# Kernel tuning notes

Hardware: AMD Instinct MI355X
Metric: run time of the kernel (lower is better)

Reference implementation:

```python
import jax, jax.numpy as jnp
import numpy as np

T, H, I, E, TOPK = 2048, 2048, 1408, 8, 2


def setup_inputs() -> dict:
    key = jax.random.key(0)
    k1, k2, k3, k4 = jax.random.split(key, 4)
    x = jax.random.normal(k1, (T, H), dtype=jnp.float32)
    router_logits = jax.random.normal(k2, (T, E), dtype=jnp.float32)
    # scale weights down so activations stay well-conditioned
    w13_weight = jax.random.normal(k3, (E, 2 * I, H), dtype=jnp.float32) * (1.0 / np.sqrt(H))
    w2_weight = jax.random.normal(k4, (E, H, I), dtype=jnp.float32) * (1.0 / np.sqrt(I))
    return {"x": x, "router_logits": router_logits, "w13_weight": w13_weight,
            "w2_weight": w2_weight, "top_k": TOPK}


def reference(x, router_logits, w13_weight, w2_weight, top_k):
    # --- select_experts: softmax scoring, top-k, renormalize ---
    probs = jax.nn.softmax(router_logits.astype(jnp.float32), axis=-1)   # [T, E]
    topk_w, topk_ids = jax.lax.top_k(probs, top_k)                        # [T, k]
    topk_w = topk_w / jnp.sum(topk_w, axis=-1, keepdims=True)             # renormalize
    topk_w = topk_w.astype(x.dtype)

    n_tok = x.shape[0]
    n_exp = w13_weight.shape[0]
    inter = w2_weight.shape[2]

    # dense combine weights [T, E]: zero for unselected experts
    comb = jnp.zeros((n_tok, n_exp), dtype=x.dtype)
    comb = comb.at[jnp.arange(n_tok)[:, None], topk_ids].add(topk_w)

    # --- fused_experts: gated SiLU MLP per expert, weighted combine ---
    gate_up = jnp.einsum('th,eih->tei', x, w13_weight)                    # [T, E, 2I]
    gate, up = gate_up[..., :inter], gate_up[..., inter:]
    act = jax.nn.silu(gate) * up                                          # [T, E, I]
    out = jnp.einsum('tei,ehi,te->th', act, w2_weight, comb)              # [T, H]
    return out
```

## Files before the change

### kernel.cpp

```cpp
#include <hip/hip_runtime.h>
#include <hip/hip_bf16.h>
#include <stdint.h>

#define T_TOK 2048
#define H_DIM 2048
#define I_DIM 1408
#define NEXP  8
#define NPOS  4096
#define NPAD  5120
#define MAXT  40

typedef short short8 __attribute__((ext_vector_type(8)));
typedef float f32x4  __attribute__((ext_vector_type(4)));

__device__ __forceinline__ short f2bf(float f) {
  union { float f; uint32_t u; } v; v.f = f;
  uint32_t r = (v.u + 0x7FFFu + ((v.u >> 16) & 1u)) >> 16;
  return (short)r;
}

__device__ __forceinline__ short8 cvt8(f32x4 a, f32x4 b) {
  __hip_bfloat162 h0 = __float22bfloat162_rn(float2{a[0], a[1]});
  __hip_bfloat162 h1 = __float22bfloat162_rn(float2{a[2], a[3]});
  __hip_bfloat162 h2 = __float22bfloat162_rn(float2{b[0], b[1]});
  __hip_bfloat162 h3 = __float22bfloat162_rn(float2{b[2], b[3]});
  short2 s0, s1, s2, s3;
  __builtin_memcpy(&s0, &h0, 4); __builtin_memcpy(&s1, &h1, 4);
  __builtin_memcpy(&s2, &h2, 4); __builtin_memcpy(&s3, &h3, 4);
  short8 r;
  r[0] = s0.x; r[1] = s0.y; r[2] = s1.x; r[3] = s1.y;
  r[4] = s2.x; r[5] = s2.y; r[6] = s3.x; r[7] = s3.y;
  return r;
}

__device__ __forceinline__ void load_lds16(const void* g, void* l) {
  __builtin_amdgcn_global_load_lds((const __attribute__((address_space(1))) uint32_t*)g,
                                   (__attribute__((address_space(3))) uint32_t*)l,
                                   16, 0, 0);
}

__global__ void k_routing(const float* __restrict__ logits,
                          int* __restrict__ pos_token,
                          float* __restrict__ pos_w,
                          int* __restrict__ eoff,
                          int* __restrict__ inv) {
  __shared__ int   s_ids[T_TOK];
  __shared__ float s_w0[T_TOK];
  __shared__ float s_w1[T_TOK];
  __shared__ int s_cnt[NEXP], s_cur[NEXP], s_off[NEXP + 1];
  const int tid = threadIdx.x;
  if (tid < NEXP) { s_cnt[tid] = 0; s_cur[tid] = 0; }
  for (int p = tid; p < NPAD; p += blockDim.x) { pos_token[p] = 0; pos_w[p] = 0.f; }
  __syncthreads();

  for (int t = tid; t < T_TOK; t += blockDim.x) {
    float l[NEXP];
#pragma unroll
    for (int e = 0; e < NEXP; ++e) l[e] = logits[t * NEXP + e];
    int b0 = 0; float v0 = l[0];
#pragma unroll
    for (int e = 1; e < NEXP; ++e) if (l[e] > v0) { v0 = l[e]; b0 = e; }
    int b1 = -1; float v1 = -1e30f;
#pragma unroll
    for (int e = 0; e < NEXP; ++e) if (e != b0 && l[e] > v1) { v1 = l[e]; b1 = e; }
    float t1 = __expf(v1 - v0);
    float w0 = 1.f / (1.f + t1);
    float w1 = 1.f - w0;
    s_ids[t] = b0 | (b1 << 8);
    s_w0[t] = w0; s_w1[t] = w1;
    atomicAdd(&s_cnt[b0], 1);
    atomicAdd(&s_cnt[b1], 1);
  }
  __syncthreads();
  if (tid == 0) {
    int acc = 0;
    for (int e = 0; e < NEXP; ++e) {
      s_off[e] = acc;
      acc += (s_cnt[e] + 127) & ~127;
    }
    s_off[NEXP] = acc;
    for (int e = 0; e <= NEXP; ++e) eoff[e] = s_off[e];
  }
  __syncthreads();
  for (int t = tid; t < T_TOK; t += blockDim.x) {
    int ids = s_ids[t];
    int e0 = ids & 255, e1 = ids >> 8;
    int p0 = s_off[e0] + atomicAdd(&s_cur[e0], 1);
    pos_token[p0] = t; pos_w[p0] = s_w0[t];
    int p1 = s_off[e1] + atomicAdd(&s_cur[e1], 1);
    pos_token[p1] = t; pos_w[p1] = s_w1[t];
    inv[2 * t] = p0; inv[2 * t + 1] = p1;
  }
}

__global__ void k_gather(const float* __restrict__ x,
                         const int* __restrict__ pos_token,
                         short* __restrict__ xg) {
  const int p = blockIdx.x;
  const int tid = threadIdx.x;
  const int tok = pos_token[p];
  const f32x4* src = (const f32x4*)(x + (size_t)tok * H_DIM);
  f32x4 a = src[tid * 2];
  f32x4 b = src[tid * 2 + 1];
  ((short8*)(xg + (size_t)p * H_DIM))[tid] = cvt8(a, b);
}

__device__ __forceinline__ int tile_expert(const int* eoff, int row0) {
  int e = 0;
#pragma unroll
  for (int i = 1; i < NEXP; ++i) if (row0 >= eoff[i]) e = i;
  return e;
}

__global__ __launch_bounds__(256, 3) void k_gateup(
    const short* __restrict__ xg, const float* __restrict__ w13,
    const int* __restrict__ eoff, short* __restrict__ act) {
  __shared__ __align__(16) short a_s[2][128 * 32];
  __shared__ __align__(16) short bg_s[2][64 * 32];
  __shared__ __align__(16) short bu_s[2][64 * 32];

  int bxr = blockIdx.x;
  const int bx = (bxr & 7) * 110 + (bxr >> 3);
  const int tile = bx / 22;
  const int nt = bx - tile * 22;
  const int row0 = tile * 128;
  if (row0 >= eoff[NEXP]) return;
  const int e = tile_expert(eoff, row0);

  const int tid = threadIdx.x;
  const int wid = tid >> 6;
  const int lane = tid & 63;
  const int wm = wid >> 1, wn = wid & 1;

  f32x4 accg[4][2] = {};
  f32x4 accu[4][2] = {};

  const short* aG  = xg + (size_t)row0 * H_DIM;
  const float* bgG = w13 + (size_t)e * (2 * I_DIM) * H_DIM + (size_t)(nt * 64) * H_DIM;
  const float* buG = bgG + (size_t)I_DIM * H_DIM;

  const int row  = tid >> 2;
  const int scol = ((tid & 3) ^ ((tid >> 3) & 3)) * 8;

  auto stageA = [&](int t, int bi) {
    const int ks = t * 32;
    load_lds16(aG + (size_t)row * H_DIM + ks + scol,        (char*)a_s[bi] + wid * 1024);
    load_lds16(aG + (size_t)(64 + row) * H_DIM + ks + scol, (char*)a_s[bi] + 4096 + wid * 1024);
  };
  auto ldB = [&](int t, f32x4& g0, f32x4& g1, f32x4& u0, f32x4& u1) {
    const int ks = t * 32;
    const float* sg = bgG + (size_t)row * H_DIM + ks + scol;
    const float* su = buG + (size_t)row * H_DIM + ks + scol;
    g0 = *(const f32x4*)sg; g1 = *(const f32x4*)(sg + 4);
    u0 = *(const f32x4*)su; u1 = *(const f32x4*)(su + 4);
  };
  auto wrB = [&](int bi, f32x4& g0, f32x4& g1, f32x4& u0, f32x4& u1) {
    *(short8*)((char*)bg_s[bi] + tid * 16) = cvt8(g0, g1);
    *(short8*)((char*)bu_s[bi] + tid * 16) = cvt8(u0, u1);
  };

  auto compute = [&](int bi) {
    const int asl = ((lane >> 4) ^ ((lane >> 1) & 3)) * 16;
    short8 af[4];
#pragma unroll
    for (int fm = 0; fm < 4; ++fm) {
      int m = wm * 64 + fm * 16 + (lane & 15);
      af[fm] = *(const short8*)((const char*)a_s[bi] + m * 64 + asl);
    }
#pragma unroll
    for (int fn = 0; fn < 2; ++fn) {
      int n = wn * 32 + fn * 16 + (lane & 15);
      short8 bg = *(const short8*)((const char*)bg_s[bi] + n * 64 + asl);
      short8 bu = *(const short8*)((const char*)bu_s[bi] + n * 64 + asl);
#pragma unroll
      for (int fm = 0; fm < 4; ++fm)
        accg[fm][fn] = __builtin_amdgcn_mfma_f32_16x16x32_bf16(af[fm], bg, accg[fm][fn], 0, 0, 0);
#pragma unroll
      for (int fm = 0; fm < 4; ++fm)
        accu[fm][fn] = __builtin_amdgcn_mfma_f32_16x16x32_bf16(af[fm], bu, accu[fm][fn], 0, 0, 0);
    }
  };

  const int NK = H_DIM / 32;
  f32x4 g0e, g1e, u0e, u1e, g0o, g1o, u0o, u1o;

  stageA(0, 0);
  ldB(0, g0e, g1e, u0e, u1e);
  wrB(0, g0e, g1e, u0e, u1e);
  ldB(1, g0e, g1e, u0e, u1e);
  ldB(2, g0o, g1o, u0o, u1o);
  __syncthreads();

#define GU_STEP(T, G0, G1, U0, U1)                                            \
  {                                                                           \
    const int t_ = (T);                                                       \
    const int bi_ = t_ & 1;                                                   \
    const int tn_ = (t_ + 1 < NK) ? t_ + 1 : NK - 1;                          \
    const int tf_ = (t_ + 3 < NK) ? t_ + 3 : NK - 1;                          \
    stageA(tn_, bi_ ^ 1);                                                     \
    __builtin_amdgcn_sched_barrier(0);                                        \
    wrB(bi_ ^ 1, G0, G1, U0, U1);                                             \
    ldB(tf_, G0, G1, U0, U1);                                                 \
    compute(bi_);                                                             \
    asm volatile("s_waitcnt vmcnt(4) lgkmcnt(0)" ::: "memory");               \
    __builtin_amdgcn_s_barrier();                                             \
  }
  for (int tp = 0; tp < NK; tp += 2) {
    GU_STEP(tp,     g0e, g1e, u0e, u1e);
    GU_STEP(tp + 1, g0o, g1o, u0o, u1o);
  }
#undef GU_STEP
  asm volatile("s_waitcnt vmcnt(0)" ::: "memory");

#pragma unroll
  for (int fm = 0; fm < 4; ++fm) {
#pragma unroll
    for (int rr = 0; rr < 4; ++rr) {
      int m = wm * 64 + fm * 16 + (lane >> 4) * 4 + rr;
      size_t grow = (size_t)(row0 + m);
#pragma unroll
      for (int fn = 0; fn < 2; ++fn) {
        int col = nt * 64 + wn * 32 + fn * 16 + (lane & 15);
        float g = accg[fm][fn][rr];
        float u = accu[fm][fn][rr];
        float a = g / (1.f + __expf(-g)) * u;
        act[grow * I_DIM + col] = f2bf(a);
      }
    }
  }
}

__global__ __launch_bounds__(256, 3) void k_down(
    const short* __restrict__ act, const float* __restrict__ w2,
    const int* __restrict__ eoff, float* __restrict__ y) {
  __shared__ __align__(16) short a_s[2][128 * 32];
  __shared__ __align__(16) short b_s[2][128 * 32];

  int bxr = blockIdx.x;
  const int bx = (bxr & 7) * 80 + (bxr >> 3);
  const int tile = bx >> 4;
  const int nt = bx & 15;
  const int row0 = tile * 128;
  if (row0 >= eoff[NEXP]) return;
  const int e = tile_expert(eoff, row0);

  const int tid = threadIdx.x;
  const int wid = tid >> 6;
  const int lane = tid & 63;
  const int wm = wid >> 1, wn = wid & 1;

  f32x4 acc[4][4] = {};

  const short* aG = act + (size_t)row0 * I_DIM;
  const float* bG = w2 + (size_t)e * H_DIM * I_DIM + (size_t)(nt * 128) * I_DIM;

  const int row  = tid >> 2;
  const int scol = ((tid & 3) ^ ((tid >> 3) & 3)) * 8;

  auto stageA = [&](int t, int bi) {
    const int ks = t * 32;
    load_lds16(aG + (size_t)row * I_DIM + ks + scol,        (char*)a_s[bi] + wid * 1024);
    load_lds16(aG + (size_t)(64 + row) * I_DIM + ks + scol, (char*)a_s[bi] + 4096 + wid * 1024);
  };
  auto ldB = [&](int t, f32x4& b00, f32x4& b01, f32x4& b10, f32x4& b11) {
    const int ks = t * 32;
    const float* s0 = bG + (size_t)row * I_DIM + ks + scol;
    const float* s1 = bG + (size_t)(64 + row) * I_DIM + ks + scol;
    b00 = *(const f32x4*)s0; b01 = *(const f32x4*)(s0 + 4);
    b10 = *(const f32x4*)s1; b11 = *(const f32x4*)(s1 + 4);
  };
  auto wrB = [&](int bi, f32x4& b00, f32x4& b01, f32x4& b10, f32x4& b11) {
    *(short8*)((char*)b_s[bi] + tid * 16)        = cvt8(b00, b01);
    *(short8*)((char*)b_s[bi] + 4096 + tid * 16) = cvt8(b10, b11);
  };

  auto compute = [&](int bi) {
    const int asl = ((lane >> 4) ^ ((lane >> 1) & 3)) * 16;
    short8 af[4];
#pragma unroll
    for (int fm = 0; fm < 4; ++fm) {
      int m = wm * 64 + fm * 16 + (lane & 15);
      af[fm] = *(const short8*)((const char*)a_s[bi] + m * 64 + asl);
    }
#pragma unroll
    for (int fn = 0; fn < 4; ++fn) {
      int n = wn * 64 + fn * 16 + (lane & 15);
      short8 bb = *(const short8*)((const char*)b_s[bi] + n * 64 + asl);
#pragma unroll
      for (int fm = 0; fm < 4; ++fm)
        acc[fm][fn] = __builtin_amdgcn_mfma_f32_16x16x32_bf16(af[fm], bb, acc[fm][fn], 0, 0, 0);
    }
  };

  const int NK = I_DIM / 32;
  f32x4 e0, e1, e2, e3, o0, o1, o2, o3;

  stageA(0, 0);
  ldB(0, e0, e1, e2, e3);
  wrB(0, e0, e1, e2, e3);
  ldB(1, e0, e1, e2, e3);
  ldB(2, o0, o1, o2, o3);
  __syncthreads();

#define DN_STEP(T, B0, B1, B2, B3)                                            \
  {                                                                           \
    const int t_ = (T);                                                       \
    const int bi_ = t_ & 1;                                                   \
    const int tn_ = (t_ + 1 < NK) ? t_ + 1 : NK - 1;                          \
    const int tf_ = (t_ + 3 < NK) ? t_ + 3 : NK - 1;                          \
    stageA(tn_, bi_ ^ 1);                                                     \
    __builtin_amdgcn_sched_barrier(0);                                        \
    wrB(bi_ ^ 1, B0, B1, B2, B3);                                             \
    ldB(tf_, B0, B1, B2, B3);                                                 \
    compute(bi_);                                                             \
    asm volatile("s_waitcnt vmcnt(4) lgkmcnt(0)" ::: "memory");               \
    __builtin_amdgcn_s_barrier();                                             \
  }
  for (int tp = 0; tp < NK; tp += 2) {
    DN_STEP(tp,     e0, e1, e2, e3);
    DN_STEP(tp + 1, o0, o1, o2, o3);
  }
#undef DN_STEP
  asm volatile("s_waitcnt vmcnt(0)" ::: "memory");

#pragma unroll
  for (int fm = 0; fm < 4; ++fm) {
#pragma unroll
    for (int rr = 0; rr < 4; ++rr) {
      int m = wm * 64 + fm * 16 + (lane >> 4) * 4 + rr;
      size_t grow = (size_t)(row0 + m);
#pragma unroll
      for (int fn = 0; fn < 4; ++fn) {
        int col = nt * 128 + wn * 64 + fn * 16 + (lane & 15);
        y[grow * H_DIM + col] = acc[fm][fn][rr];
      }
    }
  }
}

__global__ void k_combine(const float* __restrict__ y,
                          const int* __restrict__ inv,
                          const float* __restrict__ pos_w,
                          float* __restrict__ out) {
  const int t = blockIdx.x;
  const int tid = threadIdx.x;
  const int p0 = inv[2 * t], p1 = inv[2 * t + 1];
  const float w0 = pos_w[p0], w1 = pos_w[p1];
  const float4* y0 = (const float4*)(y + (size_t)p0 * H_DIM);
  const float4* y1 = (const float4*)(y + (size_t)p1 * H_DIM);
  float4* o = (float4*)(out + (size_t)t * H_DIM);
#pragma unroll
  for (int i = 0; i < 2; ++i) {
    float4 a = y0[tid * 2 + i];
    float4 b = y1[tid * 2 + i];
    float4 r;
    r.x = w0 * a.x + w1 * b.x;
    r.y = w0 * a.y + w1 * b.y;
    r.z = w0 * a.z + w1 * b.z;
    r.w = w0 * a.w + w1 * b.w;
    o[tid * 2 + i] = r;
  }
}

extern "C" void kernel_launch(void* const* d_in, const int* in_sizes, int n_in,
                              void* d_out, int out_size, void* d_ws, size_t ws_size,
                              hipStream_t stream) {
  const float* x      = (const float*)d_in[0];
  const float* logits = (const float*)d_in[1];
  const float* w13    = (const float*)d_in[2];
  const float* w2     = (const float*)d_in[3];
  (void)in_sizes; (void)n_in; (void)out_size; (void)ws_size;
  float* out = (float*)d_out;
  char* ws = (char*)d_ws;

  size_t o = 0;
  auto alloc = [&](size_t bytes) { size_t r = o; o += (bytes + 255) & ~(size_t)255; return r; };
  short* xg        = (short*)(ws + alloc((size_t)NPAD * H_DIM * 2));
  short* act       = (short*)(ws + alloc((size_t)NPAD * I_DIM * 2));
  float* y         = (float*)(ws + alloc((size_t)NPAD * H_DIM * 4));
  int*   pos_token = (int*)  (ws + alloc((size_t)NPAD * 4));
  float* pos_w     = (float*)(ws + alloc((size_t)NPAD * 4));
  int*   inv       = (int*)  (ws + alloc((size_t)T_TOK * 2 * 4));
  int*   eoff      = (int*)  (ws + alloc((NEXP + 1) * 4));

  k_routing<<<1, 1024, 0, stream>>>(logits, pos_token, pos_w, eoff, inv);
  k_gather<<<NPAD, 256, 0, stream>>>(x, pos_token, xg);
  k_gateup<<<MAXT * 22, 256, 0, stream>>>(xg, w13, eoff, act);
  k_down<<<MAXT * 16, 256, 0, stream>>>(act, w2, eoff, y);
  k_combine<<<T_TOK, 256, 0, stream>>>(y, inv, pos_w, out);
}
```

Before: 216.0 us.

## Triple-buffer A tiles with two-stage prefetch and regroup block-to-tile mapping

Both MoE GEMM kernels now keep three LDS buffers for the activation (A) tile and issue its direct-to-LDS loads two k-steps ahead instead of one, relaxing the vmcnt wait so more global loads stay in flight. This targets exposed latency on the A-tile loads. The block-index mapping is also changed so each group of eight consecutive blocks shares an n-tile across five row tiles, aiming at better L2 reuse of weight tiles. The cost is extra LDS per block, which may reduce occupancy, and the modulo-3 buffer indexing adds address arithmetic.

Result: slower. 237.0 us (+9.7%).

```diff
diff --git a/kernel.cpp b/kernel.cpp
--- a/kernel.cpp
+++ b/kernel.cpp
@@ -115,14 +115,15 @@
 __global__ __launch_bounds__(256, 3) void k_gateup(
     const short* __restrict__ xg, const float* __restrict__ w13,
     const int* __restrict__ eoff, short* __restrict__ act) {
-  __shared__ __align__(16) short a_s[2][128 * 32];
+  __shared__ __align__(16) short a_s[3][128 * 32];
   __shared__ __align__(16) short bg_s[2][64 * 32];
   __shared__ __align__(16) short bu_s[2][64 * 32];
 
-  int bxr = blockIdx.x;
-  const int bx = (bxr & 7) * 110 + (bxr >> 3);
-  const int tile = bx / 22;
-  const int nt = bx - tile * 22;
+  const int bxr = blockIdx.x;
+  const int c = bxr & 7;
+  const int l = bxr >> 3;
+  const int nt = l / 5;
+  const int tile = c * 5 + (l % 5);
   const int row0 = tile * 128;
   if (row0 >= eoff[NEXP]) return;
   const int e = tile_expert(eoff, row0);
@@ -142,10 +143,10 @@
   const int row  = tid >> 2;
   const int scol = ((tid & 3) ^ ((tid >> 3) & 3)) * 8;
 
-  auto stageA = [&](int t, int bi) {
+  auto stageA = [&](int t, int ai) {
     const int ks = t * 32;
-    load_lds16(aG + (size_t)row * H_DIM + ks + scol,        (char*)a_s[bi] + wid * 1024);
-    load_lds16(aG + (size_t)(64 + row) * H_DIM + ks + scol, (char*)a_s[bi] + 4096 + wid * 1024);
+    load_lds16(aG + (size_t)row * H_DIM + ks + scol,        (char*)a_s[ai] + wid * 1024);
+    load_lds16(aG + (size_t)(64 + row) * H_DIM + ks + scol, (char*)a_s[ai] + 4096 + wid * 1024);
   };
   auto ldB = [&](int t, f32x4& g0, f32x4& g1, f32x4& u0, f32x4& u1) {
     const int ks = t * 32;
@@ -159,13 +160,13 @@
     *(short8*)((char*)bu_s[bi] + tid * 16) = cvt8(u0, u1);
   };
 
-  auto compute = [&](int bi) {
+  auto compute = [&](int ai, int bi) {
     const int asl = ((lane >> 4) ^ ((lane >> 1) & 3)) * 16;
     short8 af[4];
 #pragma unroll
     for (int fm = 0; fm < 4; ++fm) {
       int m = wm * 64 + fm * 16 + (lane & 15);
-      af[fm] = *(const short8*)((const char*)a_s[bi] + m * 64 + asl);
+      af[fm] = *(const short8*)((const char*)a_s[ai] + m * 64 + asl);
     }
 #pragma unroll
     for (int fn = 0; fn < 2; ++fn) {
@@ -187,27 +188,29 @@
   stageA(0, 0);
   ldB(0, g0e, g1e, u0e, u1e);
   wrB(0, g0e, g1e, u0e, u1e);
-  ldB(1, g0e, g1e, u0e, u1e);
-  ldB(2, g0o, g1o, u0o, u1o);
+  stageA(1, 1);
+  ldB(1, g0o, g1o, u0o, u1o);
+  ldB(2, g0e, g1e, u0e, u1e);
   __syncthreads();
 
 #define GU_STEP(T, G0, G1, U0, U1)                                            \
   {                                                                           \
     const int t_ = (T);                                                       \
+    const int ai_ = t_ % 3;                                                   \
     const int bi_ = t_ & 1;                                                   \
-    const int tn_ = (t_ + 1 < NK) ? t_ + 1 : NK - 1;                          \
+    const int ta_ = (t_ + 2 < NK) ? t_ + 2 : NK - 1;                          \
     const int tf_ = (t_ + 3 < NK) ? t_ + 3 : NK - 1;                          \
-    stageA(tn_, bi_ ^ 1);                                                     \
+    stageA(ta_, (t_ + 2) % 3);                                                \
     __builtin_amdgcn_sched_barrier(0);                                        \
     wrB(bi_ ^ 1, G0, G1, U0, U1);                                             \
     ldB(tf_, G0, G1, U0, U1);                                                 \
-    compute(bi_);                                                             \
-    asm volatile("s_waitcnt vmcnt(4) lgkmcnt(0)" ::: "memory");               \
+    compute(ai_, bi_);                                                        \
+    asm volatile("s_waitcnt vmcnt(6) lgkmcnt(0)" ::: "memory");               \
     __builtin_amdgcn_s_barrier();                                             \
   }
   for (int tp = 0; tp < NK; tp += 2) {
-    GU_STEP(tp,     g0e, g1e, u0e, u1e);
-    GU_STEP(tp + 1, g0o, g1o, u0o, u1o);
+    GU_STEP(tp,     g0o, g1o, u0o, u1o);
+    GU_STEP(tp + 1, g0e, g1e, u0e, u1e);
   }
 #undef GU_STEP
   asm volatile("s_waitcnt vmcnt(0)" ::: "memory");
@@ -233,13 +236,14 @@
 __global__ __launch_bounds__(256, 3) void k_down(
     const short* __restrict__ act, const float* __restrict__ w2,
     const int* __restrict__ eoff, float* __restrict__ y) {
-  __shared__ __align__(16) short a_s[2][128 * 32];
+  __shared__ __align__(16) short a_s[3][128 * 32];
   __shared__ __align__(16) short b_s[2][128 * 32];
 
-  int bxr = blockIdx.x;
-  const int bx = (bxr & 7) * 80 + (bxr >> 3);
-  const int tile = bx >> 4;
-  const int nt = bx & 15;
+  const int bxr = blockIdx.x;
+  const int c = bxr & 7;
+  const int l = bxr >> 3;
+  const int nt = l / 5;
+  const int tile = c * 5 + (l % 5);
   const int row0 = tile * 128;
   if (row0 >= eoff[NEXP]) return;
   const int e = tile_expert(eoff, row0);
@@ -257,10 +261,10 @@
   const int row  = tid >> 2;
   const int scol = ((tid & 3) ^ ((tid >> 3) & 3)) * 8;
 
-  auto stageA = [&](int t, int bi) {
+  auto stageA = [&](int t, int ai) {
     const int ks = t * 32;
-    load_lds16(aG + (size_t)row * I_DIM + ks + scol,        (char*)a_s[bi] + wid * 1024);
-    load_lds16(aG + (size_t)(64 + row) * I_DIM + ks + scol, (char*)a_s[bi] + 4096 + wid * 1024);
+    load_lds16(aG + (size_t)row * I_DIM + ks + scol,        (char*)a_s[ai] + wid * 1024);
+    load_lds16(aG + (size_t)(64 + row) * I_DIM + ks + scol, (char*)a_s[ai] + 4096 + wid * 1024);
   };
   auto ldB = [&](int t, f32x4& b00, f32x4& b01, f32x4& b10, f32x4& b11) {
     const int ks = t * 32;
@@ -274,13 +278,13 @@
     *(short8*)((char*)b_s[bi] + 4096 + tid * 16) = cvt8(b10, b11);
   };
 
-  auto compute = [&](int bi) {
+  auto compute = [&](int ai, int bi) {
     const int asl = ((lane >> 4) ^ ((lane >> 1) & 3)) * 16;
     short8 af[4];
 #pragma unroll
     for (int fm = 0; fm < 4; ++fm) {
       int m = wm * 64 + fm * 16 + (lane & 15);
-      af[fm] = *(const short8*)((const char*)a_s[bi] + m * 64 + asl);
+      af[fm] = *(const short8*)((const char*)a_s[ai] + m * 64 + asl);
     }
 #pragma unroll
     for (int fn = 0; fn < 4; ++fn) {
@@ -298,27 +302,29 @@
   stageA(0, 0);
   ldB(0, e0, e1, e2, e3);
   wrB(0, e0, e1, e2, e3);
-  ldB(1, e0, e1, e2, e3);
-  ldB(2, o0, o1, o2, o3);
+  stageA(1, 1);
+  ldB(1, o0, o1, o2, o3);
+  ldB(2, e0, e1, e2, e3);
   __syncthreads();
 
 #define DN_STEP(T, B0, B1, B2, B3)                                            \
   {                                                                           \
     const int t_ = (T);                                                       \
+    const int ai_ = t_ % 3;                                                   \
     const int bi_ = t_ & 1;                                                   \
-    const int tn_ = (t_ + 1 < NK) ? t_ + 1 : NK - 1;                          \
+    const int ta_ = (t_ + 2 < NK) ? t_ + 2 : NK - 1;                          \
     const int tf_ = (t_ + 3 < NK) ? t_ + 3 : NK - 1;                          \
-    stageA(tn_, bi_ ^ 1);                                                     \
+    stageA(ta_, (t_ + 2) % 3);                                                \
     __builtin_amdgcn_sched_barrier(0);                                        \
     wrB(bi_ ^ 1, B0, B1, B2, B3);                                             \
     ldB(tf_, B0, B1, B2, B3);                                                 \
-    compute(bi_);                                                             \
-    asm volatile("s_waitcnt vmcnt(4) lgkmcnt(0)" ::: "memory");               \
+    compute(ai_, bi_);                                                        \
+    asm volatile("s_waitcnt vmcnt(6) lgkmcnt(0)" ::: "memory");               \
     __builtin_amdgcn_s_barrier();                                             \
   }
   for (int tp = 0; tp < NK; tp += 2) {
-    DN_STEP(tp,     e0, e1, e2, e3);
-    DN_STEP(tp + 1, o0, o1, o2, o3);
+    DN_STEP(tp,     o0, o1, o2, o3);
+    DN_STEP(tp + 1, e0, e1, e2, e3);
   }
 #undef DN_STEP
   asm volatile("s_waitcnt vmcnt(0)" ::: "memory");
```

## Process two row tiles per gate-up block and simplify the prefetch pipeline

Applied to the files above, without the earlier changes.

The gate-up kernel now launches half as many blocks, and each block loops over two consecutive 128-row tiles while keeping the same weight column slice, so the block count roughly matches a single wave of CUs. The deep register prefetch of B three steps ahead, with manual waitcnt and s_barrier, is replaced by a plain one-step double buffer using __syncthreads. The aim is less tail imbalance and some weight reuse in L2 within a block. The cost is less latency hiding in the main loop, and tiles that span two experts load a different weight slice per half.

New measurement: 250.6 us. 1.16x slower.

```diff
diff --git a/kernel.cpp b/kernel.cpp
--- a/kernel.cpp
+++ b/kernel.cpp
@@ -5,10 +5,12 @@
 #define T_TOK 2048
 #define H_DIM 2048
 #define I_DIM 1408
+#define GU_W  2816
 #define NEXP  8
 #define NPOS  4096
 #define NPAD  5120
 #define MAXT  40
+#define NPAIR 20
 
 typedef short short8 __attribute__((ext_vector_type(8)));
 typedef float f32x4  __attribute__((ext_vector_type(4)));
@@ -120,113 +122,100 @@
   __shared__ __align__(16) short bu_s[2][64 * 32];
 
   int bxr = blockIdx.x;
-  const int bx = (bxr & 7) * 110 + (bxr >> 3);
-  const int tile = bx / 22;
-  const int nt = bx - tile * 22;
-  const int row0 = tile * 128;
-  if (row0 >= eoff[NEXP]) return;
-  const int e = tile_expert(eoff, row0);
+  const int bx = (bxr & 7) * 55 + (bxr >> 3);
+  const int c  = bx / 22;
+  const int nt = bx - c * 22;
 
   const int tid = threadIdx.x;
   const int wid = tid >> 6;
   const int lane = tid & 63;
   const int wm = wid >> 1, wn = wid & 1;
 
-  f32x4 accg[4][2] = {};
-  f32x4 accu[4][2] = {};
-
-  const short* aG  = xg + (size_t)row0 * H_DIM;
-  const float* bgG = w13 + (size_t)e * (2 * I_DIM) * H_DIM + (size_t)(nt * 64) * H_DIM;
-  const float* buG = bgG + (size_t)I_DIM * H_DIM;
-
   const int row  = tid >> 2;
   const int scol = ((tid & 3) ^ ((tid >> 3) & 3)) * 8;
 
-  auto stageA = [&](int t, int bi) {
-    const int ks = t * 32;
-    load_lds16(aG + (size_t)row * H_DIM + ks + scol,        (char*)a_s[bi] + wid * 1024);
-    load_lds16(aG + (size_t)(64 + row) * H_DIM + ks + scol, (char*)a_s[bi] + 4096 + wid * 1024);
-  };
-  auto ldB = [&](int t, f32x4& g0, f32x4& g1, f32x4& u0, f32x4& u1) {
-    const int ks = t * 32;
-    const float* sg = bgG + (size_t)row * H_DIM + ks + scol;
-    const float* su = buG + (size_t)row * H_DIM + ks + scol;
-    g0 = *(const f32x4*)sg; g1 = *(const f32x4*)(sg + 4);
-    u0 = *(const f32x4*)su; u1 = *(const f32x4*)(su + 4);
-  };
-  auto wrB = [&](int bi, f32x4& g0, f32x4& g1, f32x4& u0, f32x4& u1) {
-    *(short8*)((char*)bg_s[bi] + tid * 16) = cvt8(g0, g1);
-    *(short8*)((char*)bu_s[bi] + tid * 16) = cvt8(u0, u1);
-  };
-
-  auto compute = [&](int bi) {
-    const int asl = ((lane >> 4) ^ ((lane >> 1) & 3)) * 16;
-    short8 af[4];
+  for (int half = 0; half < 2; ++half) {
+    const int tile = c * 2 + half;
+    const int row0 = tile * 128;
+    if (row0 >= eoff[NEXP]) break;
+    const int e = tile_expert(eoff, row0);
+
+    f32x4 accg[4][2] = {};
+    f32x4 accu[4][2] = {};
+
+    const short* aG  = xg + (size_t)row0 * H_DIM;
+    const float* bgG = w13 + (size_t)e * GU_W * H_DIM + (size_t)(nt * 64) * H_DIM;
+    const float* buG = bgG + (size_t)I_DIM * H_DIM;
+
+    auto stageA = [&](int t, int bi) {
+      const int ks = t * 32;
+      load_lds16(aG + (size_t)row * H_DIM + ks + scol,        (char*)a_s[bi] + wid * 1024);
+      load_lds16(aG + (size_t)(64 + row) * H_DIM + ks + scol, (char*)a_s[bi] + 4096 + wid * 1024);
+    };
+
+    f32x4 g0, g1, u0, u1;
+    auto ldB = [&](int t) {
+      const int ks = t * 32;
+      const float* sg = bgG + (size_t)row * H_DIM + ks + scol;
+      const float* su = buG + (size_t)row * H_DIM + ks + scol;
+      g0 = *(const f32x4*)sg; g1 = *(const f32x4*)(sg + 4);
+      u0 = *(const f32x4*)su; u1 = *(const f32x4*)(su + 4);
+    };
+    auto wrB = [&](int bi) {
+      *(short8*)((char*)bg_s[bi] + tid * 16) = cvt8(g0, g1);
+      *(short8*)((char*)bu_s[bi] + tid * 16) = cvt8(u0, u1);
+    };
+
+    auto compute = [&](int bi) {
+      const int asl = ((lane >> 4) ^ ((lane >> 1) & 3)) * 16;
+      short8 af[4];
+#pragma unroll
+      for (int fm = 0; fm < 4; ++fm) {
+        int m = wm * 64 + fm * 16 + (lane & 15);
+        af[fm] = *(const short8*)((const char*)a_s[bi] + m * 64 + asl);
+      }
+#pragma unroll
+      for (int fn = 0; fn < 2; ++fn) {
+        int n = wn * 32 + fn * 16 + (lane & 15);
+        short8 bg = *(const short8*)((const char*)bg_s[bi] + n * 64 + asl);
+        short8 bu = *(const short8*)((const char*)bu_s[bi] + n * 64 + asl);
+#pragma unroll
+        for (int fm = 0; fm < 4; ++fm)
+          accg[fm][fn] = __builtin_amdgcn_mfma_f32_16x16x32_bf16(af[fm], bg, accg[fm][fn], 0, 0, 0);
+#pragma unroll
+        for (int fm = 0; fm < 4; ++fm)
+          accu[fm][fn] = __builtin_amdgcn_mfma_f32_16x16x32_bf16(af[fm], bu, accu[fm][fn], 0, 0, 0);
+      }
+    };
+
+    const int NK = H_DIM / 32;
+    stageA(0, 0); ldB(0); wrB(0);
+    __syncthreads();
+    for (int t = 0; t < NK; ++t) {
+      int bi = t & 1;
+      if (t + 1 < NK) { stageA(t + 1, bi ^ 1); ldB(t + 1); }
+      compute(bi);
+      if (t + 1 < NK) wrB(bi ^ 1);
+      __syncthreads();
+    }
+
 #pragma unroll
     for (int fm = 0; fm < 4; ++fm) {
-      int m = wm * 64 + fm * 16 + (lane & 15);
-      af[fm] = *(const short8*)((const char*)a_s[bi] + m * 64 + asl);
-    }
-#pragma unroll
-    for (int fn = 0; fn < 2; ++fn) {
-      int n = wn * 32 + fn * 16 + (lane & 15);
-      short8 bg = *(const short8*)((const char*)bg_s[bi] + n * 64 + asl);
-      short8 bu = *(const short8*)((const char*)bu_s[bi] + n * 64 + asl);
-#pragma unroll
-      for (int fm = 0; fm < 4; ++fm)
-        accg[fm][fn] = __builtin_amdgcn_mfma_f32_16x16x32_bf16(af[fm], bg, accg[fm][fn], 0, 0, 0);
-#pragma unroll
-      for (int fm = 0; fm < 4; ++fm)
-        accu[fm][fn] = __builtin_amdgcn_mfma_f32_16x16x32_bf16(af[fm], bu, accu[fm][fn], 0, 0, 0);
-    }
-  };
-
-  const int NK = H_DIM / 32;
-  f32x4 g0e, g1e, u0e, u1e, g0o, g1o, u0o, u1o;
-
-  stageA(0, 0);
-  ldB(0, g0e, g1e, u0e, u1e);
-  wrB(0, g0e, g1e, u0e, u1e);
-  ldB(1, g0e, g1e, u0e, u1e);
-  ldB(2, g0o, g1o, u0o, u1o);
-  __syncthreads();
-
-#define GU_STEP(T, G0, G1, U0, U1)                                            \
-  {                                                                           \
-    const int t_ = (T);                                                       \
-    const int bi_ = t_ & 1;                                                   \
-    const int tn_ = (t_ + 1 < NK) ? t_ + 1 : NK - 1;                          \
-    const int tf_ = (t_ + 3 < NK) ? t_ + 3 : NK - 1;                          \
-    stageA(tn_, bi_ ^ 1);                                                     \
-    __builtin_amdgcn_sched_barrier(0);                                        \
-    wrB(bi_ ^ 1, G0, G1, U0, U1);                                             \
-    ldB(tf_, G0, G1, U0, U1);                                                 \
-    compute(bi_);                                                             \
-    asm volatile("s_waitcnt vmcnt(4) lgkmcnt(0)" ::: "memory");               \
-    __builtin_amdgcn_s_barrier();                                             \
-  }
-  for (int tp = 0; tp < NK; tp += 2) {
-    GU_STEP(tp,     g0e, g1e, u0e, u1e);
-    GU_STEP(tp + 1, g0o, g1o, u0o, u1o);
-  }
-#undef GU_STEP
-  asm volatile("s_waitcnt vmcnt(0)" ::: "memory");
-
-#pragma unroll
-  for (int fm = 0; fm < 4; ++fm) {
-#pragma unroll
-    for (int rr = 0; rr < 4; ++rr) {
-      int m = wm * 64 + fm * 16 + (lane >> 4) * 4 + rr;
-      size_t grow = (size_t)(row0 + m);
-#pragma unroll
-      for (int fn = 0; fn < 2; ++fn) {
-        int col = nt * 64 + wn * 32 + fn * 16 + (lane & 15);
-        float g = accg[fm][fn][rr];
-        float u = accu[fm][fn][rr];
-        float a = g / (1.f + __expf(-g)) * u;
-        act[grow * I_DIM + col] = f2bf(a);
+#pragma unroll
+      for (int rr = 0; rr < 4; ++rr) {
+        int m = wm * 64 + fm * 16 + (lane >> 4) * 4 + rr;
+        size_t grow = (size_t)(row0 + m);
+#pragma unroll
+        for (int fn = 0; fn < 2; ++fn) {
+          int col = nt * 64 + wn * 32 + fn * 16 + (lane & 15);
+          float g = accg[fm][fn][rr];
+          float u = accu[fm][fn][rr];
+          float a = g / (1.f + __expf(-g)) * u;
+          act[grow * I_DIM + col] = f2bf(a);
+        }
       }
     }
+    __syncthreads();
   }
 }
 
@@ -385,7 +374,7 @@
 
   k_routing<<<1, 1024, 0, stream>>>(logits, pos_token, pos_w, eoff, inv);
   k_gather<<<NPAD, 256, 0, stream>>>(x, pos_token, xg);
-  k_gateup<<<MAXT * 22, 256, 0, stream>>>(xg, w13, eoff, act);
+  k_gateup<<<NPAIR * 22, 256, 0, stream>>>(xg, w13, eoff, act);
   k_down<<<MAXT * 16, 256, 0, stream>>>(act, w2, eoff, y);
   k_combine<<<T_TOK, 256, 0, stream>>>(y, inv, pos_w, out);
 }
```
